# Optimization experiments

Measured on AMD Instinct MI355X. Metric: run time of the kernel, lower is better.

## Reference

```python
import jax, jax.numpy as jnp
import numpy as np

V, E, H, L, C, B, T = 50000, 1024, 512, 2, 24, 32, 512


def _lstm_layer(x, Wih, Whh, bih, bhh):
    # x: [T, B, D]; PyTorch gate order i, f, g, o stacked along 4H.
    Hh = Whh.shape[1]
    Bb = x.shape[1]
    bias = bih + bhh

    def step(carry, xt):
        h, c = carry
        g = xt @ Wih.T + h @ Whh.T + bias  # [B, 4H]
        i, f, gg, o = jnp.split(g, 4, axis=-1)
        i = jax.nn.sigmoid(i)
        f = jax.nn.sigmoid(f)
        gg = jnp.tanh(gg)
        o = jax.nn.sigmoid(o)
        c = f * c + i * gg
        h = o * jnp.tanh(c)
        return (h, c), h

    init = (jnp.zeros((Bb, Hh), x.dtype), jnp.zeros((Bb, Hh), x.dtype))
    _, hs = jax.lax.scan(step, init, x)
    return hs  # [T, B, H]


def _bilstm(x, w_ih, w_hh, b_ih, b_hh):
    # stacked weights: [L, 2(dir), 4H, D] / [L, 2, 4H, H] / [L, 2, 4H]
    out = x
    for l in range(w_ih.shape[0]):
        fwd = _lstm_layer(out, w_ih[l, 0], w_hh[l, 0], b_ih[l, 0], b_hh[l, 0])
        bwd = _lstm_layer(out[::-1], w_ih[l, 1], w_hh[l, 1], b_ih[l, 1], b_hh[l, 1])[::-1]
        out = jnp.concatenate([fwd, bwd], axis=-1)
    return out  # [T, B, 2H]


def _crf_llh(em, tags, start, end, trans):
    # em: [T, B, C], tags: [T, B]; torchcrf log-likelihood, reduction='sum', full mask.
    # numerator: score of the gold tag path
    em_sc = jnp.take_along_axis(em, tags[:, :, None], axis=2)[:, :, 0].sum(0)  # [B]
    tr_sc = trans[tags[:-1], tags[1:]].sum(0)  # [B]
    num = start[tags[0]] + em_sc + tr_sc + end[tags[-1]]

    # denominator: forward algorithm (logsumexp DP over tag dim)
    def step(alpha, em_t):
        nxt = jax.nn.logsumexp(alpha[:, :, None] + trans[None, :, :] + em_t[:, None, :], axis=1)
        return nxt, None

    alpha0 = start[None, :] + em[0]  # [B, C]
    alphaT, _ = jax.lax.scan(step, alpha0, em[1:])
    logZ = jax.nn.logsumexp(alphaT + end[None, :], axis=1)  # [B]
    return jnp.sum(num - logZ)


def setup_inputs() -> dict:
    key = jax.random.key(0)
    ks = jax.random.split(key, 12)
    k = 1.0 / np.sqrt(H)  # PyTorch LSTM/Linear init scale
    u = lambda kk, shp, s: jax.random.uniform(kk, shp, jnp.float32, -s, s)
    return {
        "x": jax.random.randint(ks[0], (B, T), 0, V),
        "labels": jax.random.randint(ks[1], (B, T), 0, C),
        "emb_table": jax.random.normal(ks[2], (V, E), jnp.float32),
        "w_ih": u(ks[3], (L, 2, 4 * H, E), k),   # E == 2H so all layers share input dim
        "w_hh": u(ks[4], (L, 2, 4 * H, H), k),
        "b_ih": u(ks[5], (L, 2, 4 * H), k),
        "b_hh": u(ks[6], (L, 2, 4 * H), k),
        "fc_w": u(ks[7], (C, 2 * H), 1.0 / np.sqrt(2 * H)),
        "fc_b": u(ks[8], (C,), 1.0 / np.sqrt(2 * H)),
        "crf_start": u(ks[9], (C,), 0.1),
        "crf_end": u(ks[10], (C,), 0.1),
        "crf_trans": u(ks[11], (C, C), 0.1),
    }


def reference(x, labels, emb_table, w_ih, w_hh, b_ih, b_hh, fc_w, fc_b, crf_start, crf_end, crf_trans):
    embed = emb_table[x]                      # [B, T, E]
    xt = jnp.transpose(embed, (1, 0, 2))      # [T, B, E]
    h = _bilstm(xt, w_ih, w_hh, b_ih, b_hh)   # [T, B, 2H] (dropout is identity in eval)
    logits = jnp.einsum('tbh,ch->tbc', h, fc_w) + fc_b  # [T, B, C]
    llh = _crf_llh(logits, jnp.transpose(labels), crf_start, crf_end, crf_trans)
    return jnp.transpose(logits, (0, 1, 2)).transpose(1, 0, 2), -llh
```

## Files before the change

### kernel.cpp

```cpp
#include <hip/hip_runtime.h>


typedef __bf16 bf16;
typedef _Float16 f16;
typedef __bf16 bf16x8 __attribute__((ext_vector_type(8)));
typedef __bf16 bf16x4 __attribute__((ext_vector_type(4)));
typedef _Float16 f16x4 __attribute__((ext_vector_type(4)));
typedef float f32x4 __attribute__((ext_vector_type(4)));
typedef unsigned int u32;
typedef unsigned long long u64;

#define TT 512
#define BB 32
#define HH 512
#define CC_ 24
#define MROWS 16384
#define KDIM 1024
#define NGATE 2048

__device__ __forceinline__ f32x4 mfma16(bf16x8 a, bf16x8 b, f32x4 c) {
  return __builtin_amdgcn_mfma_f32_16x16x32_bf16(a, b, c, 0, 0, 0);
}
__device__ __forceinline__ float sigmoidf_(float x) { return 1.f / (1.f + __expf(-x)); }
__device__ __forceinline__ float tanhf_(float x) {
  float e = __expf(2.f * x);
  return 1.f - 2.f / (e + 1.f);
}

__global__ __launch_bounds__(256) void convert_w_k(
    const float* __restrict__ wih, const float* __restrict__ whh, const float* __restrict__ fcw,
    bf16* __restrict__ wihb, bf16* __restrict__ whhb, bf16* __restrict__ fcwb) {
  const int n1 = (2 * 2 * NGATE * KDIM) / 4;
  const int n2 = (2 * 2 * NGATE * HH) / 4;
  const int n3 = (32 * KDIM) / 4;
  int stride = gridDim.x * blockDim.x;
  for (int i = blockIdx.x * blockDim.x + threadIdx.x; i < n1 + n2 + n3; i += stride) {
    float4 v;
    bf16* dst;
    if (i < n1) {
      v = ((const float4*)wih)[i];
      dst = wihb + (size_t)i * 4;
    } else if (i < n1 + n2) {
      int j = i - n1;
      v = ((const float4*)whh)[j];
      dst = whhb + (size_t)j * 4;
    } else {
      int j = i - n1 - n2;
      if ((j >> 8) < CC_) v = ((const float4*)fcw)[j];
      else                v = make_float4(0.f, 0.f, 0.f, 0.f);
      dst = fcwb + (size_t)j * 4;
    }
    bf16x4 o; o[0] = (bf16)v.x; o[1] = (bf16)v.y; o[2] = (bf16)v.z; o[3] = (bf16)v.w;
    *(bf16x4*)dst = o;
  }
}

__global__ __launch_bounds__(64) void embed_k(const int* __restrict__ x,
                                              const float* __restrict__ emb,
                                              bf16* __restrict__ xt) {
  int row = blockIdx.x;
  int t = row >> 5, b = row & 31;
  int tok = x[b * TT + t];
  const float4* src = (const float4*)(emb + (size_t)tok * KDIM);
  bf16* dst = xt + (size_t)row * KDIM;
  int i = threadIdx.x;
#pragma unroll
  for (int c = 0; c < 4; ++c) {
    float4 v = src[i + 64 * c];
    bf16x4 o; o[0] = (bf16)v.x; o[1] = (bf16)v.y; o[2] = (bf16)v.z; o[3] = (bf16)v.w;
    *(bf16x4*)(dst + (size_t)(i + 64 * c) * 4) = o;
  }
}

__global__ __launch_bounds__(256, 2) void gemm_in_k(
    const bf16* __restrict__ A, const bf16* __restrict__ W,
    const float* __restrict__ bih, const float* __restrict__ bhh,
    f16* __restrict__ Gh) {
  __shared__ bf16 As[128 * 72];
  __shared__ bf16 Ws[128 * 72];
  int dir = blockIdx.z;
  const bf16* Wd = W + (size_t)dir * NGATE * KDIM;
  const float* bi = bih + dir * NGATE;
  const float* bh = bhh + dir * NGATE;
  f16* G = Gh + (size_t)dir * 64 * MROWS * 32;
  int m0 = blockIdx.y * 128;
  int n0 = blockIdx.x * 128;
  int tid = threadIdx.x;
  int lane = tid & 63, wave = tid >> 6;
  int wm = wave >> 1, wn = wave & 1;
  int cn = lane & 15, quad = lane >> 4;

  f32x4 zz = {0.f, 0.f, 0.f, 0.f};
  f32x4 acc[4][4];
#pragma unroll
  for (int a = 0; a < 4; ++a)
#pragma unroll
    for (int b = 0; b < 4; ++b) acc[a][b] = zz;

  for (int k0 = 0; k0 < KDIM; k0 += 64) {
    __syncthreads();
#pragma unroll
    for (int j = 0; j < 4; ++j) {
      int cch = tid + 256 * j;
      int row = cch >> 3, kq = cch & 7;
      *(bf16x8*)&As[row * 72 + kq * 8] =
          *(const bf16x8*)&A[(size_t)(m0 + row) * KDIM + k0 + kq * 8];
      *(bf16x8*)&Ws[row * 72 + kq * 8] =
          *(const bf16x8*)&Wd[(size_t)(n0 + row) * KDIM + k0 + kq * 8];
    }
    __syncthreads();
#pragma unroll
    for (int kc = 0; kc < 2; ++kc) {
      bf16x8 af[4], bw[4];
#pragma unroll
      for (int mt = 0; mt < 4; ++mt)
        af[mt] = *(const bf16x8*)&As[(wm * 64 + mt * 16 + cn) * 72 + kc * 32 + quad * 8];
#pragma unroll
      for (int nt = 0; nt < 4; ++nt)
        bw[nt] = *(const bf16x8*)&Ws[(wn * 64 + nt * 16 + cn) * 72 + kc * 32 + quad * 8];
#pragma unroll
      for (int mt = 0; mt < 4; ++mt)
#pragma unroll
        for (int nt = 0; nt < 4; ++nt)
          acc[mt][nt] = mfma16(af[mt], bw[nt], acc[mt][nt]);
    }
  }
#pragma unroll
  for (int nt = 0; nt < 4; ++nt) {
    int n = n0 + wn * 64 + nt * 16 + cn;
    float bias = bi[n] + bh[n];
    int col = n & 511, gate = n >> 9;
    size_t base = (size_t)(col >> 3) * MROWS * 32 + (size_t)(col & 7) * 4 + gate;
#pragma unroll
    for (int mt = 0; mt < 4; ++mt) {
#pragma unroll
      for (int r = 0; r < 4; ++r) {
        int row = m0 + wm * 64 + mt * 16 + quad * 4 + r;
        G[base + (size_t)row * 32] = (f16)(acc[mt][nt][r] + bias);
      }
    }
  }
}

__global__ __launch_bounds__(64) void rec_k(
    const f16* __restrict__ Gin,
    const bf16* __restrict__ Whh,
    bf16* __restrict__ hbuf,
    u64* __restrict__ hx,
    u32* __restrict__ flags) {
  int wg = blockIdx.x;
  int dir = blockIdx.y;
  int lane = threadIdx.x;
  int cn = lane & 15, quad = lane >> 4;
  int j0 = wg * 8;
  const bf16* Wd = Whh + (size_t)dir * NGATE * HH;
  const f16* Gw = Gin + ((size_t)dir * 64 + wg) * MROWS * 32;
  u64* hxd = hx + (size_t)dir * TT * 4096;
  u32* fl = flags + (size_t)dir * TT * 64;

  __shared__ bf16 Bl[2 * 16 * 520];
  __shared__ bf16 hS[32][8];
  for (int c = lane; c < 2 * 16 * 64; c += 64) {
    int col = c >> 6;
    int kc8 = c & 63;
    int nt = col >> 4, ccn = col & 15;
    int gate = nt * 2 + (ccn >> 3);
    int jj_ = ccn & 7;
    int n = gate * HH + j0 + jj_;
    *(bf16x8*)&Bl[col * 520 + kc8 * 8] = *(const bf16x8*)&Wd[(size_t)n * HH + kc8 * 8];
  }
  __syncthreads();

  float cst[2][4];
#pragma unroll
  for (int mt = 0; mt < 2; ++mt)
#pragma unroll
    for (int r = 0; r < 4; ++r) cst[mt][r] = 0.f;
  bool active = cn < 8;
  int jj = cn & 7;
  f32x4 zz = {0.f, 0.f, 0.f, 0.f};

  int pb = lane >> 1, half = lane & 1;
  int sIdx = (j0 >> 5) * 256 + (((pb >= 16) ? 2 : 0) + half) * 64 +
             ((j0 >> 3) & 3) * 16 + (pb & 15);
  size_t hbOff = ((size_t)pb * KDIM + dir * HH + j0 + half * 4);

  for (int s = 0; s < TT; ++s) {
    int t = dir ? (TT - 1 - s) : s;
    f16x4 gp_[2][4];
    if (active) {
#pragma unroll
      for (int mt = 0; mt < 2; ++mt)
#pragma unroll
        for (int r = 0; r < 4; ++r) {
          int b = mt * 16 + quad * 4 + r;
          gp_[mt][r] = *(const f16x4*)&Gw[(size_t)(t * BB + b) * 32 + jj * 4];
        }
    }
    f32x4 acc[2][2];
    acc[0][0] = zz; acc[0][1] = zz; acc[1][0] = zz; acc[1][1] = zz;
    if (s > 0) {
      int tp = dir ? (t + 1) : (t - 1);
      u32* f = fl + (size_t)(s - 1) * 64;
      while (__hip_atomic_load(&f[lane], __ATOMIC_RELAXED, __HIP_MEMORY_SCOPE_AGENT) == 0u)
        __builtin_amdgcn_s_sleep(1);
      asm volatile("s_waitcnt vmcnt(0)" ::: "memory");
      const u64* hb8 = hxd + (size_t)tp * 4096;
#pragma unroll 4
      for (int kk = 0; kk < 16; ++kk) {
        union { u64 u[2]; bf16x8 v; } a0, a1;
        a0.u[0] = __hip_atomic_load(&hb8[kk * 256 + lane],       __ATOMIC_RELAXED, __HIP_MEMORY_SCOPE_AGENT);
        a0.u[1] = __hip_atomic_load(&hb8[kk * 256 + 64 + lane],  __ATOMIC_RELAXED, __HIP_MEMORY_SCOPE_AGENT);
        a1.u[0] = __hip_atomic_load(&hb8[kk * 256 + 128 + lane], __ATOMIC_RELAXED, __HIP_MEMORY_SCOPE_AGENT);
        a1.u[1] = __hip_atomic_load(&hb8[kk * 256 + 192 + lane], __ATOMIC_RELAXED, __HIP_MEMORY_SCOPE_AGENT);
        bf16x8 b0 = *(const bf16x8*)&Bl[(0 * 16 + cn) * 520 + kk * 32 + quad * 8];
        bf16x8 b1 = *(const bf16x8*)&Bl[(1 * 16 + cn) * 520 + kk * 32 + quad * 8];
        acc[0][0] = mfma16(a0.v, b0, acc[0][0]);
        acc[0][1] = mfma16(a0.v, b1, acc[0][1]);
        acc[1][0] = mfma16(a1.v, b0, acc[1][0]);
        acc[1][1] = mfma16(a1.v, b1, acc[1][1]);
      }
    }
#pragma unroll
    for (int mt = 0; mt < 2; ++mt) {
#pragma unroll
      for (int r = 0; r < 4; ++r) {
        float ip = acc[mt][0][r], gp = acc[mt][1][r];
        float fp = __shfl(ip, lane + 8);
        float op = __shfl(gp, lane + 8);
        if (active) {
          float xi = ip + (float)gp_[mt][r][0];
          float xf = fp + (float)gp_[mt][r][1];
          float xg = gp + (float)gp_[mt][r][2];
          float xo = op + (float)gp_[mt][r][3];
          float it = sigmoidf_(xi);
          float ft = sigmoidf_(xf);
          float gt = tanhf_(xg);
          float ot = sigmoidf_(xo);
          float cc = ft * cst[mt][r] + it * gt;
          cst[mt][r] = cc;
          int b = mt * 16 + quad * 4 + r;
          hS[b][jj] = (bf16)(ot * tanhf_(cc));
        }
      }
    }
    __syncthreads();
    u64 pv = *(const u64*)&hS[pb][half * 4];
    __hip_atomic_store(&hxd[(size_t)t * 4096 + sIdx], pv, __ATOMIC_RELAXED,
                       __HIP_MEMORY_SCOPE_AGENT);
    *(u64*)&hbuf[(size_t)(t * BB) * KDIM + hbOff] = pv;
    asm volatile("s_waitcnt vmcnt(0)" ::: "memory");
    if (lane == 0)
      __hip_atomic_store(&fl[(size_t)s * 64 + wg], 1u, __ATOMIC_RELAXED,
                         __HIP_MEMORY_SCOPE_AGENT);
  }
}

__global__ __launch_bounds__(64) void gemm_fc_k(
    const bf16* __restrict__ hbuf,
    const bf16* __restrict__ fcw,
    const float* __restrict__ fcb,
    float* __restrict__ outp) {
  int m0 = blockIdx.x * 16;
  int lane = threadIdx.x;
  int cn = lane & 15, quad = lane >> 4;
  f32x4 acc0 = {0.f, 0.f, 0.f, 0.f}, acc1 = {0.f, 0.f, 0.f, 0.f};
  for (int k0 = 0; k0 < KDIM; k0 += 32) {
    bf16x8 a  = *(const bf16x8*)&hbuf[(size_t)(m0 + cn) * KDIM + k0 + quad * 8];
    bf16x8 b0 = *(const bf16x8*)&fcw[(size_t)cn * KDIM + k0 + quad * 8];
    bf16x8 b1 = *(const bf16x8*)&fcw[(size_t)(cn + 16) * KDIM + k0 + quad * 8];
    acc0 = mfma16(a, b0, acc0);
    acc1 = mfma16(a, b1, acc1);
  }
#pragma unroll
  for (int r = 0; r < 4; ++r) {
    int row = m0 + quad * 4 + r;
    int t = row >> 5, b = row & 31;
    float* o = outp + (size_t)b * (TT * CC_) + (size_t)t * CC_;
    o[cn] = acc0[r] + fcb[cn];
    int c1 = cn + 16;
    if (c1 < CC_) o[c1] = acc1[r] + fcb[c1];
  }
  if (blockIdx.x == 0 && lane == 0) outp[(size_t)BB * TT * CC_] = 0.f;
}

__global__ __launch_bounds__(64) void crf_k(
    const float* __restrict__ em,
    const int* __restrict__ labels,
    const float* __restrict__ start_, const float* __restrict__ end_,
    const float* __restrict__ trans, float* __restrict__ result) {
  int b = blockIdx.x;
  int j = threadIdx.x;
  bool act = j < CC_;
  int jc = act ? j : 0;
  float tcol[CC_];
#pragma unroll
  for (int i = 0; i < CC_; ++i) tcol[i] = trans[i * CC_ + jc];
  const float* emb_ = em + (size_t)b * (TT * CC_);
  float alpha = act ? (start_[jc] + emb_[jc]) : -1e30f;
  for (int t = 1; t < TT; ++t) {
    float m = -1e30f;
#pragma unroll
    for (int i = 0; i < CC_; ++i) {
      float ai = __shfl(alpha, i);
      m = fmaxf(m, ai + tcol[i]);
    }
    float ssum = 0.f;
#pragma unroll
    for (int i = 0; i < CC_; ++i) {
      float ai = __shfl(alpha, i);
      ssum += __expf(ai + tcol[i] - m);
    }
    float na = m + __logf(ssum) + emb_[(size_t)t * CC_ + jc];
    alpha = act ? na : -1e30f;
  }
  float v = act ? (alpha + end_[jc]) : -1e30f;
  float mm = v;
#pragma unroll
  for (int off = 32; off; off >>= 1) mm = fmaxf(mm, __shfl_xor(mm, off));
  float e = act ? __expf(v - mm) : 0.f;
#pragma unroll
  for (int off = 32; off; off >>= 1) e += __shfl_xor(e, off);
  float logZ = mm + __logf(e);
  float part = 0.f;
  for (int t = j; t < TT; t += 64) {
    int tag = labels[b * TT + t];
    part += emb_[(size_t)t * CC_ + tag];
    if (t < TT - 1) part += trans[tag * CC_ + labels[b * TT + t + 1]];
  }
#pragma unroll
  for (int off = 32; off; off >>= 1) part += __shfl_xor(part, off);
  if (j == 0) {
    float num = part + start_[labels[b * TT]] + end_[labels[b * TT + TT - 1]];
    atomicAdd(result, logZ - num);
  }
}

extern "C" void kernel_launch(void* const* d_in, const int* in_sizes, int n_in,
                              void* d_out, int out_size, void* d_ws, size_t ws_size,
                              hipStream_t stream) {
  const int*   x      = (const int*)d_in[0];
  const int*   labels = (const int*)d_in[1];
  const float* emb    = (const float*)d_in[2];
  const float* w_ih   = (const float*)d_in[3];
  const float* w_hh   = (const float*)d_in[4];
  const float* b_ih   = (const float*)d_in[5];
  const float* b_hh   = (const float*)d_in[6];
  const float* fc_w   = (const float*)d_in[7];
  const float* fc_b   = (const float*)d_in[8];
  const float* crf_s  = (const float*)d_in[9];
  const float* crf_e  = (const float*)d_in[10];
  const float* crf_t  = (const float*)d_in[11];
  float* out = (float*)d_out;
  (void)in_sizes; (void)n_in; (void)out_size; (void)ws_size;

  char* ws = (char*)d_ws;
  bf16* xt    = (bf16*)ws;
  bf16* h0    = (bf16*)(ws + 33554432);
  bf16* h1    = (bf16*)(ws + 67108864);
  bf16* wihb  = (bf16*)(ws + 100663296);
  bf16* whhb  = (bf16*)(ws + 117440512);
  bf16* fcwb  = (bf16*)(ws + 125829120);
  f16*  gin   = (f16*)(ws + 125894656);
  u64*  hx    = (u64*)(ws + 260112384);
  u32*  flags = (u32*)(ws + 293666816);

  hipMemsetAsync(flags, 0, 2 * 2 * TT * 64 * sizeof(u32), stream);
  convert_w_k<<<2048, 256, 0, stream>>>(w_ih, w_hh, fc_w, wihb, whhb, fcwb);
  embed_k<<<MROWS, 64, 0, stream>>>(x, emb, xt);

  gemm_in_k<<<dim3(16, 128, 2), 256, 0, stream>>>(xt, wihb, b_ih, b_hh, gin);
  rec_k<<<dim3(64, 2), 64, 0, stream>>>(gin, whhb, h0, hx, flags);
  gemm_in_k<<<dim3(16, 128, 2), 256, 0, stream>>>(
      h0, wihb + (size_t)2 * NGATE * KDIM, b_ih + 2 * NGATE, b_hh + 2 * NGATE, gin);
  rec_k<<<dim3(64, 2), 64, 0, stream>>>(
      gin, whhb + (size_t)2 * NGATE * HH, h1, hx, flags + 2 * TT * 64);

  gemm_fc_k<<<MROWS / 16, 64, 0, stream>>>(h1, fcwb, fc_b, out);
  crf_k<<<BB, 64, 0, stream>>>(out, labels, crf_s, crf_e, crf_t,
                               out + (size_t)BB * TT * CC_);
}
```

Baseline: 9.717 ms.

## Place recurrent workgroups on a single XCC to sync through its local L2

The recurrent kernel now launches 2048 workgroups. Each one reads its XCC ID and claims a slot, and the first XCC to gather 128 workgroups wins. Only that XCC's 128 workgroups run the LSTM recurrence. Flags and h-exchange then use plain or workgroup-scope accesses that stay in the shared L2, avoiding agent-scope coherent traffic across XCCs. There is a timeout fallback to the original agent-scope path. Gate pre-activation loads are also prefetched one step ahead. The risks are that correctness depends on same-XCC L2 coherence assumptions, plus the launch overhead of the extra workgroups.

```diff
diff --git a/kernel.cpp b/kernel.cpp
--- a/kernel.cpp
+++ b/kernel.cpp
@@ -142,15 +142,12 @@
   }
 }
 
-__global__ __launch_bounds__(64) void rec_k(
-    const f16* __restrict__ Gin,
-    const bf16* __restrict__ Whh,
-    bf16* __restrict__ hbuf,
-    u64* __restrict__ hx,
-    u32* __restrict__ flags) {
-  int wg = blockIdx.x;
-  int dir = blockIdx.y;
-  int lane = threadIdx.x;
+template <bool LOCAL>
+__device__ __forceinline__ void rec_loop(
+    int dir, int wg, int lane,
+    const f16* __restrict__ Gin, const bf16* __restrict__ Whh,
+    bf16* __restrict__ hbuf, u64* __restrict__ hx, u32* __restrict__ flags,
+    bf16* __restrict__ Bl, bf16 (*__restrict__ hS)[8]) {
   int cn = lane & 15, quad = lane >> 4;
   int j0 = wg * 8;
   const bf16* Wd = Whh + (size_t)dir * NGATE * HH;
@@ -158,8 +155,6 @@
   u64* hxd = hx + (size_t)dir * TT * 4096;
   u32* fl = flags + (size_t)dir * TT * 64;
 
-  __shared__ bf16 Bl[2 * 16 * 520];
-  __shared__ bf16 hS[32][8];
   for (int c = lane; c < 2 * 16 * 64; c += 64) {
     int col = c >> 6;
     int kc8 = c & 63;
@@ -185,34 +180,56 @@
              ((j0 >> 3) & 3) * 16 + (pb & 15);
   size_t hbOff = ((size_t)pb * KDIM + dir * HH + j0 + half * 4);
 
+  u32 zero = 0;
+  asm volatile("" : "+v"(zero));
+
+  f16x4 gpn[2][4];
+  {
+    int t0 = dir ? (TT - 1) : 0;
+    if (active) {
+#pragma unroll
+      for (int mt = 0; mt < 2; ++mt)
+#pragma unroll
+        for (int r = 0; r < 4; ++r) {
+          int b = mt * 16 + quad * 4 + r;
+          gpn[mt][r] = *(const f16x4*)&Gw[(size_t)(t0 * BB + b) * 32 + jj * 4];
+        }
+    }
+  }
+
   for (int s = 0; s < TT; ++s) {
     int t = dir ? (TT - 1 - s) : s;
-    f16x4 gp_[2][4];
-    if (active) {
-#pragma unroll
-      for (int mt = 0; mt < 2; ++mt)
-#pragma unroll
-        for (int r = 0; r < 4; ++r) {
-          int b = mt * 16 + quad * 4 + r;
-          gp_[mt][r] = *(const f16x4*)&Gw[(size_t)(t * BB + b) * 32 + jj * 4];
-        }
-    }
     f32x4 acc[2][2];
     acc[0][0] = zz; acc[0][1] = zz; acc[1][0] = zz; acc[1][1] = zz;
     if (s > 0) {
       int tp = dir ? (t + 1) : (t - 1);
       u32* f = fl + (size_t)(s - 1) * 64;
-      while (__hip_atomic_load(&f[lane], __ATOMIC_RELAXED, __HIP_MEMORY_SCOPE_AGENT) == 0u)
+      for (;;) {
+        u32 v;
+        if constexpr (LOCAL)
+          v = __hip_atomic_fetch_or(&f[lane], zero, __ATOMIC_RELAXED,
+                                    __HIP_MEMORY_SCOPE_WORKGROUP);
+        else
+          v = __hip_atomic_load(&f[lane], __ATOMIC_RELAXED, __HIP_MEMORY_SCOPE_AGENT);
+        if (__all(v != 0u)) break;
         __builtin_amdgcn_s_sleep(1);
+      }
       asm volatile("s_waitcnt vmcnt(0)" ::: "memory");
       const u64* hb8 = hxd + (size_t)tp * 4096;
 #pragma unroll 4
       for (int kk = 0; kk < 16; ++kk) {
         union { u64 u[2]; bf16x8 v; } a0, a1;
-        a0.u[0] = __hip_atomic_load(&hb8[kk * 256 + lane],       __ATOMIC_RELAXED, __HIP_MEMORY_SCOPE_AGENT);
-        a0.u[1] = __hip_atomic_load(&hb8[kk * 256 + 64 + lane],  __ATOMIC_RELAXED, __HIP_MEMORY_SCOPE_AGENT);
-        a1.u[0] = __hip_atomic_load(&hb8[kk * 256 + 128 + lane], __ATOMIC_RELAXED, __HIP_MEMORY_SCOPE_AGENT);
-        a1.u[1] = __hip_atomic_load(&hb8[kk * 256 + 192 + lane], __ATOMIC_RELAXED, __HIP_MEMORY_SCOPE_AGENT);
+        if constexpr (LOCAL) {
+          a0.u[0] = hb8[kk * 256 + lane];
+          a0.u[1] = hb8[kk * 256 + 64 + lane];
+          a1.u[0] = hb8[kk * 256 + 128 + lane];
+          a1.u[1] = hb8[kk * 256 + 192 + lane];
+        } else {
+          a0.u[0] = __hip_atomic_load(&hb8[kk * 256 + lane],       __ATOMIC_RELAXED, __HIP_MEMORY_SCOPE_AGENT);
+          a0.u[1] = __hip_atomic_load(&hb8[kk * 256 + 64 + lane],  __ATOMIC_RELAXED, __HIP_MEMORY_SCOPE_AGENT);
+          a1.u[0] = __hip_atomic_load(&hb8[kk * 256 + 128 + lane], __ATOMIC_RELAXED, __HIP_MEMORY_SCOPE_AGENT);
+          a1.u[1] = __hip_atomic_load(&hb8[kk * 256 + 192 + lane], __ATOMIC_RELAXED, __HIP_MEMORY_SCOPE_AGENT);
+        }
         bf16x8 b0 = *(const bf16x8*)&Bl[(0 * 16 + cn) * 520 + kk * 32 + quad * 8];
         bf16x8 b1 = *(const bf16x8*)&Bl[(1 * 16 + cn) * 520 + kk * 32 + quad * 8];
         acc[0][0] = mfma16(a0.v, b0, acc[0][0]);
@@ -229,10 +246,10 @@
         float fp = __shfl(ip, lane + 8);
         float op = __shfl(gp, lane + 8);
         if (active) {
-          float xi = ip + (float)gp_[mt][r][0];
-          float xf = fp + (float)gp_[mt][r][1];
-          float xg = gp + (float)gp_[mt][r][2];
-          float xo = op + (float)gp_[mt][r][3];
+          float xi = ip + (float)gpn[mt][r][0];
+          float xf = fp + (float)gpn[mt][r][1];
+          float xg = gp + (float)gpn[mt][r][2];
+          float xo = op + (float)gpn[mt][r][3];
           float it = sigmoidf_(xi);
           float ft = sigmoidf_(xf);
           float gt = tanhf_(xg);
@@ -246,14 +263,81 @@
     }
     __syncthreads();
     u64 pv = *(const u64*)&hS[pb][half * 4];
-    __hip_atomic_store(&hxd[(size_t)t * 4096 + sIdx], pv, __ATOMIC_RELAXED,
-                       __HIP_MEMORY_SCOPE_AGENT);
+    if constexpr (LOCAL)
+      hxd[(size_t)t * 4096 + sIdx] = pv;
+    else
+      __hip_atomic_store(&hxd[(size_t)t * 4096 + sIdx], pv, __ATOMIC_RELAXED,
+                         __HIP_MEMORY_SCOPE_AGENT);
     *(u64*)&hbuf[(size_t)(t * BB) * KDIM + hbOff] = pv;
     asm volatile("s_waitcnt vmcnt(0)" ::: "memory");
-    if (lane == 0)
-      __hip_atomic_store(&fl[(size_t)s * 64 + wg], 1u, __ATOMIC_RELAXED,
-                         __HIP_MEMORY_SCOPE_AGENT);
-  }
+    if (lane == 0) {
+      if constexpr (LOCAL)
+        fl[(size_t)s * 64 + wg] = 1u;
+      else
+        __hip_atomic_store(&fl[(size_t)s * 64 + wg], 1u, __ATOMIC_RELAXED,
+                           __HIP_MEMORY_SCOPE_AGENT);
+    }
+    int tn = dir ? (t - 1) : (t + 1);
+    if (active) {
+#pragma unroll
+      for (int mt = 0; mt < 2; ++mt)
+#pragma unroll
+        for (int r = 0; r < 4; ++r) {
+          int b = mt * 16 + quad * 4 + r;
+          gpn[mt][r] = *(const f16x4*)&Gw[(size_t)(tn * BB + b) * 32 + jj * 4];
+        }
+    }
+  }
+}
+
+__global__ __launch_bounds__(64) void rec_k(
+    const f16* __restrict__ Gin,
+    const bf16* __restrict__ Whh,
+    bf16* __restrict__ hbuf,
+    u64* __restrict__ hx,
+    u32* __restrict__ flags,
+    u32* __restrict__ claim) {
+  __shared__ bf16 Bl[2 * 16 * 520];
+  __shared__ bf16 hS[32][8];
+  int lane = threadIdx.x;
+
+  u32 xcc;
+  asm volatile("s_getreg_b32 %0, hwreg(HW_REG_XCC_ID)" : "=s"(xcc));
+  xcc &= 7u;
+  u32 idx = 0;
+  if (lane == 0) idx = atomicAdd(&claim[xcc], 1u);
+  idx = (u32)__shfl((int)idx, 0);
+  if (idx >= 128u) return;
+  if (idx == 127u && lane == 0) atomicCAS(&claim[8], 0u, xcc + 1u);
+
+  u32 w;
+  u64 t0 = __builtin_amdgcn_s_memrealtime();
+  for (;;) {
+    w = __hip_atomic_load(&claim[8], __ATOMIC_RELAXED, __HIP_MEMORY_SCOPE_AGENT);
+    if (w != 0u) break;
+    if (__builtin_amdgcn_s_memrealtime() - t0 > 300000ull) {
+      if (lane == 0) atomicCAS(&claim[8], 0u, 0xFFFFu);
+    }
+    __builtin_amdgcn_s_sleep(8);
+  }
+
+  int role;
+  bool local;
+  if (w == 0xFFFFu) {
+    u32 r = 0;
+    if (lane == 0) r = atomicAdd(&claim[9], 1u);
+    r = (u32)__shfl((int)r, 0);
+    if (r >= 128u) return;
+    role = (int)r; local = false;
+  } else {
+    if (w != xcc + 1u) return;
+    role = (int)idx; local = true;
+  }
+  int dir = (role >> 2) & 1;
+  int wg  = ((role >> 3) << 2) | (role & 3);
+
+  if (local) rec_loop<true >(dir, wg, lane, Gin, Whh, hbuf, hx, flags, Bl, hS);
+  else       rec_loop<false>(dir, wg, lane, Gin, Whh, hbuf, hx, flags, Bl, hS);
 }
 
 __global__ __launch_bounds__(64) void gemm_fc_k(
@@ -364,17 +448,19 @@
   f16*  gin   = (f16*)(ws + 125894656);
   u64*  hx    = (u64*)(ws + 260112384);
   u32*  flags = (u32*)(ws + 293666816);
+  u32*  claim = (u32*)xt;
 
   hipMemsetAsync(flags, 0, 2 * 2 * TT * 64 * sizeof(u32), stream);
   convert_w_k<<<2048, 256, 0, stream>>>(w_ih, w_hh, fc_w, wihb, whhb, fcwb);
   embed_k<<<MROWS, 64, 0, stream>>>(x, emb, xt);
 
   gemm_in_k<<<dim3(16, 128, 2), 256, 0, stream>>>(xt, wihb, b_ih, b_hh, gin);
-  rec_k<<<dim3(64, 2), 64, 0, stream>>>(gin, whhb, h0, hx, flags);
+  hipMemsetAsync(claim, 0, 128, stream);
+  rec_k<<<2048, 64, 0, stream>>>(gin, whhb, h0, hx, flags, claim);
   gemm_in_k<<<dim3(16, 128, 2), 256, 0, stream>>>(
       h0, wihb + (size_t)2 * NGATE * KDIM, b_ih + 2 * NGATE, b_hh + 2 * NGATE, gin);
-  rec_k<<<dim3(64, 2), 64, 0, stream>>>(
-      gin, whhb + (size_t)2 * NGATE * HH, h1, hx, flags + 2 * TT * 64);
+  rec_k<<<2048, 64, 0, stream>>>(
+      gin, whhb + (size_t)2 * NGATE * HH, h1, hx, flags + 2 * TT * 64, claim + 16);
 
   gemm_fc_k<<<MROWS / 16, 64, 0, stream>>>(h1, fcwb, fc_b, out);
   crf_k<<<BB, 64, 0, stream>>>(out, labels, crf_s, crf_e, crf_t,
```

Result: slower. 14.57 ms (+50.0%).
